# Performance work log

Hardware: AMD Instinct MI355X
Metric: run time of the kernel (lower is better)

## Reference

```python
import jax, jax.numpy as jnp
import numpy as np

N_NODES = 50000
N_EDGES = 800000
F = 128
LN_EPS = 1e-5


def _sage_conv(h, src, dst, Wl, bl, Wr, n_nodes):
    # PyG SAGEConv (aggr='mean', root_weight=True):
    #   out_i = lin_l(mean_{j->i} h_j) + lin_r(h_i)
    msg = h[src]  # [E, F] irregular gather
    s = jax.ops.segment_sum(msg, dst, num_segments=n_nodes)  # [N, F]
    deg = jax.ops.segment_sum(jnp.ones((src.shape[0],), h.dtype), dst,
                              num_segments=n_nodes)  # [N]
    mean = s / jnp.maximum(deg, 1.0)[:, None]
    return mean @ Wl.T + bl + h @ Wr.T


def _graph_layernorm(h, w, b):
    # PyG LayerNorm mode='graph', batch=None: normalize over ALL entries,
    # eps added to std, then per-channel affine.
    m = h.mean()
    std = jnp.sqrt(jnp.mean((h - m) ** 2))
    return (h - m) / (std + LN_EPS) * w + b


def _prelu(h, w):
    # nn.PReLU(1): single shared slope
    return jnp.where(h >= 0, h, w * h)


def setup_inputs() -> dict:
    key = jax.random.key(0)
    ks = jax.random.split(key, 12)
    sc = 1.0 / np.sqrt(F)
    x = jax.random.normal(ks[0], (N_NODES, F), dtype=jnp.float32)
    edge_index = jax.random.randint(ks[1], (2, N_EDGES), 0, N_NODES, dtype=jnp.int64)
    return {
        "x": x,
        "edge_index": edge_index,
        "Wl0": jax.random.uniform(ks[2], (F, F), jnp.float32, -sc, sc),
        "bl0": jnp.zeros((F,), jnp.float32),
        "Wr0": jax.random.uniform(ks[3], (F, F), jnp.float32, -sc, sc),
        "ln_w0": jnp.ones((F,), jnp.float32),
        "ln_b0": jnp.zeros((F,), jnp.float32),
        "pw0": jnp.full((1,), 0.25, jnp.float32),
        "skipW0": jax.random.uniform(ks[4], (F, F), jnp.float32, -sc, sc),
        "Wl1": jax.random.uniform(ks[5], (F, F), jnp.float32, -sc, sc),
        "bl1": jnp.zeros((F,), jnp.float32),
        "Wr1": jax.random.uniform(ks[6], (F, F), jnp.float32, -sc, sc),
        "ln_w1": jnp.ones((F,), jnp.float32),
        "ln_b1": jnp.zeros((F,), jnp.float32),
        "pw1": jnp.full((1,), 0.25, jnp.float32),
    }


def reference(x, edge_index, Wl0, bl0, Wr0, ln_w0, ln_b0, pw0, skipW0,
              Wl1, bl1, Wr1, ln_w1, ln_b1, pw1):
    src, dst = edge_index[0], edge_index[1]
    n = x.shape[0]
    # layer 0: h = x
    h = _sage_conv(x, src, dst, Wl0, bl0, Wr0, n)
    h = _graph_layernorm(h, ln_w0, ln_b0)
    h1 = _prelu(h, pw0)
    # layer 1: h = skip(x) + h1
    h = x @ skipW0.T + h1
    h = _sage_conv(h, src, dst, Wl1, bl1, Wr1, n)
    h = _graph_layernorm(h, ln_w1, ln_b1)
    h = _prelu(h, pw1)
    return h
```

## Files before the change

kernel.cpp:

```cpp
#include <hip/hip_runtime.h>

#define LN_EPS 1e-5f
#define BUCKCAP 4096
#define PCHUNK 6656
#define PK 13

typedef short bf16x8 __attribute__((ext_vector_type(8)));
typedef float f32x4  __attribute__((ext_vector_type(4)));

static __device__ __forceinline__ float4 ld4(const float* p){ return *(const float4*)p; }
static __device__ __forceinline__ uint f2bf1(float f){
  uint u = __float_as_uint(f);
  return (u + 0x7fffu + ((u >> 16) & 1u)) >> 16;
}
static __device__ __forceinline__ float bf2f(uint lo16){ return __uint_as_float(lo16 << 16); }

__global__ void detect_fmt_kernel(const int* __restrict__ ei, int* __restrict__ flag){
  __shared__ int any;
  if (threadIdx.x == 0) any = 0;
  __syncthreads();
  int nz = 0;
  for (int i = threadIdx.x; i < 1024; i += 256)
    nz |= (ei[2*i+1] != 0);
  if (nz) atomicOr(&any, 1);
  __syncthreads();
  if (threadIdx.x == 0) *flag = any;
}

__global__ __launch_bounds__(512) void partition_kernel(
    const int* __restrict__ ei, int E, const int* __restrict__ flag,
    int* __restrict__ bucket_count, uint* __restrict__ ebuf, int nbuck){
  __shared__ int hist[512];
  __shared__ int base[512];
  __shared__ int cur[512];
  const int tid = threadIdx.x;
  const int lo = blockIdx.x * PCHUNK;
  const int hi = min(lo + PCHUNK, E);
  hist[tid] = 0;
  __syncthreads();

  const int fmt = *flag;
  uint pd[PK];
  #pragma unroll
  for (int k = 0; k < PK; k++){
    int e = lo + tid + k*512;
    uint v = 0xffffffffu;
    if (e < hi){
      int s, d;
      if (fmt){ s = ei[e]; d = ei[E + e]; }
      else    { s = ei[2*e]; d = ei[2*(E + e)]; }
      v = ((uint)d << 16) | (uint)s;
      atomicAdd(&hist[v >> 23], 1);
    }
    pd[k] = v;
  }
  __syncthreads();
  { int h = hist[tid];
    base[tid] = (h > 0 && tid < nbuck) ? atomicAdd(&bucket_count[tid], h) : 0;
    cur[tid] = 0; }
  __syncthreads();
  #pragma unroll
  for (int k = 0; k < PK; k++){
    int e = lo + tid + k*512;
    if (e < hi){
      uint v = pd[k];
      int b = v >> 23;
      int pos = base[b] + atomicAdd(&cur[b], 1);
      if (pos < BUCKCAP) ebuf[(size_t)b*BUCKCAP + pos] = v;
    }
  }
}

__global__ void convert_bf16_kernel(const float* __restrict__ src, ushort* __restrict__ dst, int n8){
  int i = blockIdx.x*256 + threadIdx.x;
  if (i >= n8) return;
  float4 a = ld4(src + (size_t)i*8);
  float4 b = ld4(src + (size_t)i*8 + 4);
  uint4 o;
  o.x = f2bf1(a.x) | (f2bf1(a.y) << 16);
  o.y = f2bf1(a.z) | (f2bf1(a.w) << 16);
  o.z = f2bf1(b.x) | (f2bf1(b.y) << 16);
  o.w = f2bf1(b.z) | (f2bf1(b.w) << 16);
  *(uint4*)(dst + (size_t)i*8) = o;
}

__global__ void convert_w_kernel(const float* __restrict__ s0, const float* __restrict__ s1,
                                 const float* __restrict__ s2, const float* __restrict__ s3,
                                 const float* __restrict__ s4, ushort* __restrict__ dst){
  int i = blockIdx.x*256 + threadIdx.x;
  if (i >= 10240) return;
  int m = i >> 11;
  int o = (i & 2047) * 8;
  const float* s = (m == 0) ? s0 : (m == 1) ? s1 : (m == 2) ? s2 : (m == 3) ? s3 : s4;
  float4 a = ld4(s + o);
  float4 b = ld4(s + o + 4);
  uint4 v;
  v.x = f2bf1(a.x) | (f2bf1(a.y) << 16);
  v.y = f2bf1(a.z) | (f2bf1(a.w) << 16);
  v.z = f2bf1(b.x) | (f2bf1(b.y) << 16);
  v.w = f2bf1(b.z) | (f2bf1(b.w) << 16);
  *(uint4*)(dst + (size_t)m*16384 + o) = v;
}

__global__ __launch_bounds__(512) void bucket_aggregate(const ushort* __restrict__ h,
    const uint* __restrict__ ebuf, const int* __restrict__ bucket_count,
    ushort* __restrict__ outmean, int N){
  __shared__ ushort ssrc[BUCKCAP];
  __shared__ int lcnt[128], lofs[128], lcur[128];
  const int tid = threadIdx.x;
  const int b = blockIdx.x;
  const int n0 = b << 7;
  const uint* eb = ebuf + (size_t)b*BUCKCAP;
  const int cnt = min(bucket_count[b], BUCKCAP);

  if (tid < 128) lcnt[tid] = 0;
  __syncthreads();
  for (int e = tid; e < cnt; e += 512)
    atomicAdd(&lcnt[(eb[e] >> 16) & 127], 1);
  __syncthreads();
  if (tid < 128){
    int v = lcnt[tid];
    int s = v;
    #pragma unroll
    for (int off = 1; off < 64; off <<= 1){
      int u = __shfl_up(s, off);
      if ((tid & 63) >= off) s += u;
    }
    lofs[tid] = s - v;
  }
  __syncthreads();
  if (tid >= 64 && tid < 128)
    lofs[tid] += lofs[63] + lcnt[63];
  __syncthreads();
  if (tid < 128) lcur[tid] = lofs[tid];
  __syncthreads();
  for (int e = tid; e < cnt; e += 512){
    uint v = eb[e];
    int pos = atomicAdd(&lcur[(v >> 16) & 127], 1);
    ssrc[pos] = (ushort)(v & 0xffffu);
  }
  __syncthreads();

  const int wv = tid >> 6, lane = tid & 63;
  const uint* hp = (const uint*)h;
  uint* op = (uint*)outmean;
  #pragma unroll 1
  for (int i = 0; i < 16; i++){
    int j = wv*16 + i;
    int node = n0 + j;
    if (node >= N) break;
    int start = lofs[j];
    int d = lcnt[j];
    float ax = 0.f, ay = 0.f;
    int e = 0;
    for (; e + 4 <= d; e += 4){
      int s0 = ssrc[start+e+0], s1 = ssrc[start+e+1];
      int s2 = ssrc[start+e+2], s3 = ssrc[start+e+3];
      uint v0 = hp[(size_t)s0*64 + lane];
      uint v1 = hp[(size_t)s1*64 + lane];
      uint v2 = hp[(size_t)s2*64 + lane];
      uint v3 = hp[(size_t)s3*64 + lane];
      ax += bf2f(v0 & 0xffffu) + bf2f(v1 & 0xffffu) + bf2f(v2 & 0xffffu) + bf2f(v3 & 0xffffu);
      ay += bf2f(v0 >> 16) + bf2f(v1 >> 16) + bf2f(v2 >> 16) + bf2f(v3 >> 16);
    }
    for (; e < d; e++){
      int s0 = ssrc[start+e];
      uint v = hp[(size_t)s0*64 + lane];
      ax += bf2f(v & 0xffffu);
      ay += bf2f(v >> 16);
    }
    float inv = 1.f / fmaxf((float)d, 1.f);
    op[(size_t)node*64 + lane] = f2bf1(ax*inv) | (f2bf1(ay*inv) << 16);
  }
}

__global__ __launch_bounds__(256) void gemm_dual_mfma(
    const ushort* __restrict__ A1, const ushort* __restrict__ A2,
    const ushort* __restrict__ W1, const ushort* __restrict__ W2,
    const float* __restrict__ bias, float* __restrict__ out,
    int N, double* __restrict__ stats){
  const int tid  = threadIdx.x;
  const int lane = tid & 63;
  const int wv   = tid >> 6;
  const int r0   = blockIdx.x*128 + wv*32;
  const int lrow = lane & 15;
  const int lk   = (lane >> 4) * 8;

  f32x4 acc[2][8] = {};

  #pragma unroll
  for (int ks = 0; ks < 4; ks++){
    const int kb = ks*32 + lk;
    bf16x8 a1[2], a2[2];
    #pragma unroll
    for (int m = 0; m < 2; m++){
      int r = r0 + m*16 + lrow;
      if (r > N-1) r = N-1;
      a1[m] = *(const bf16x8*)(A1 + (size_t)r*128 + kb);
      a2[m] = *(const bf16x8*)(A2 + (size_t)r*128 + kb);
    }
    #pragma unroll
    for (int n = 0; n < 8; n++){
      const int c = n*16 + lrow;
      bf16x8 b1 = *(const bf16x8*)(W1 + c*128 + kb);
      bf16x8 b2 = *(const bf16x8*)(W2 + c*128 + kb);
      #pragma unroll
      for (int m = 0; m < 2; m++){
        acc[m][n] = __builtin_amdgcn_mfma_f32_16x16x32_bf16(a1[m], b1, acc[m][n], 0, 0, 0);
        acc[m][n] = __builtin_amdgcn_mfma_f32_16x16x32_bf16(a2[m], b2, acc[m][n], 0, 0, 0);
      }
    }
  }

  float bn[8];
  #pragma unroll
  for (int n = 0; n < 8; n++) bn[n] = bias[n*16 + lrow];

  double ls1 = 0.0, ls2 = 0.0;
  const int rb = (lane >> 4) * 4;
  #pragma unroll
  for (int m = 0; m < 2; m++){
    #pragma unroll
    for (int j = 0; j < 4; j++){
      int r = r0 + m*16 + rb + j;
      if (r < N){
        #pragma unroll
        for (int n = 0; n < 8; n++){
          float v = acc[m][n][j] + bn[n];
          out[(size_t)r*128 + n*16 + lrow] = v;
          ls1 += (double)v;
          ls2 += (double)v * (double)v;
        }
      }
    }
  }
  #pragma unroll
  for (int off = 32; off > 0; off >>= 1){
    ls1 += __shfl_down(ls1, off);
    ls2 += __shfl_down(ls2, off);
  }
  __shared__ double red[8];
  if (lane == 0){ red[wv*2] = ls1; red[wv*2+1] = ls2; }
  __syncthreads();
  if (tid == 0) atomicAdd(&stats[0], red[0]+red[2]+red[4]+red[6]);
  if (tid == 1) atomicAdd(&stats[1], red[1]+red[3]+red[5]+red[7]);
}

__global__ __launch_bounds__(256) void gemm_skip_mfma(
    const ushort* __restrict__ A, const ushort* __restrict__ W,
    const float* __restrict__ T0, const double* __restrict__ stats,
    const float* __restrict__ lnw, const float* __restrict__ lnb,
    const float* __restrict__ pw,
    ushort* __restrict__ outb, int N, double inv_cnt){
  const int tid  = threadIdx.x;
  const int lane = tid & 63;
  const int wv   = tid >> 6;
  const int r0   = blockIdx.x*128 + wv*32;
  const int lrow = lane & 15;
  const int lk   = (lane >> 4) * 8;

  f32x4 acc[2][8] = {};

  #pragma unroll
  for (int ks = 0; ks < 4; ks++){
    const int kb = ks*32 + lk;
    bf16x8 a[2];
    #pragma unroll
    for (int m = 0; m < 2; m++){
      int r = r0 + m*16 + lrow;
      if (r > N-1) r = N-1;
      a[m] = *(const bf16x8*)(A + (size_t)r*128 + kb);
    }
    #pragma unroll
    for (int n = 0; n < 8; n++){
      const int c = n*16 + lrow;
      bf16x8 b = *(const bf16x8*)(W + c*128 + kb);
      #pragma unroll
      for (int m = 0; m < 2; m++)
        acc[m][n] = __builtin_amdgcn_mfma_f32_16x16x32_bf16(a[m], b, acc[m][n], 0, 0, 0);
    }
  }

  double s1 = stats[0], s2 = stats[1];
  double md = s1 * inv_cnt;
  double var = s2 * inv_cnt - md*md;
  float mean = (float)md;
  float rstd = 1.f / ((float)sqrt(fmax(var, 0.0)) + LN_EPS);
  float slope = pw[0];
  float wn[8], bb[8];
  #pragma unroll
  for (int n = 0; n < 8; n++){
    wn[n] = lnw[n*16 + lrow];
    bb[n] = lnb[n*16 + lrow];
  }

  const int rb = (lane >> 4) * 4;
  #pragma unroll
  for (int m = 0; m < 2; m++){
    #pragma unroll
    for (int j = 0; j < 4; j++){
      int r = r0 + m*16 + rb + j;
      if (r < N){
        #pragma unroll
        for (int n = 0; n < 8; n++){
          float t = T0[(size_t)r*128 + n*16 + lrow];
          float l = (t - mean)*rstd*wn[n] + bb[n];
          l = (l >= 0.f) ? l : slope*l;
          float v = acc[m][n][j] + l;
          outb[(size_t)r*128 + n*16 + lrow] = (ushort)f2bf1(v);
        }
      }
    }
  }
}

__global__ __launch_bounds__(256) void ln_prelu_kernel(
    const float* __restrict__ T, const double* __restrict__ stats,
    const float* __restrict__ lnw, const float* __restrict__ lnb,
    const float* __restrict__ pw, float* __restrict__ out,
    int nf4, double inv_cnt){
  double s1 = stats[0], s2 = stats[1];
  double md = s1 * inv_cnt;
  double var = s2 * inv_cnt - md*md;
  float mean = (float)md;
  float rstd = 1.f / ((float)sqrt(fmax(var, 0.0)) + LN_EPS);
  float slope = pw[0];
  for (int i = blockIdx.x*256 + threadIdx.x; i < nf4; i += gridDim.x*256){
    int c4 = i & 31;
    float4 t = ld4(T + (size_t)i*4);
    float4 w4 = ld4(lnw + c4*4);
    float4 b4 = ld4(lnb + c4*4);
    float4 v; float l;
    l = (t.x - mean)*rstd*w4.x + b4.x; v.x = (l >= 0.f ? l : slope*l);
    l = (t.y - mean)*rstd*w4.y + b4.y; v.y = (l >= 0.f ? l : slope*l);
    l = (t.z - mean)*rstd*w4.z + b4.z; v.z = (l >= 0.f ? l : slope*l);
    l = (t.w - mean)*rstd*w4.w + b4.w; v.w = (l >= 0.f ? l : slope*l);
    *(float4*)(out + (size_t)i*4) = v;
  }
}

extern "C" void kernel_launch(void* const* d_in, const int* in_sizes, int n_in,
                              void* d_out, int out_size, void* d_ws, size_t ws_size,
                              hipStream_t stream){
  const float* x    = (const float*)d_in[0];
  const int*   ei   = (const int*)d_in[1];
  const float* Wl0  = (const float*)d_in[2];
  const float* bl0  = (const float*)d_in[3];
  const float* Wr0  = (const float*)d_in[4];
  const float* lnw0 = (const float*)d_in[5];
  const float* lnb0 = (const float*)d_in[6];
  const float* pw0  = (const float*)d_in[7];
  const float* skW  = (const float*)d_in[8];
  const float* Wl1  = (const float*)d_in[9];
  const float* bl1  = (const float*)d_in[10];
  const float* Wr1  = (const float*)d_in[11];
  const float* lnw1 = (const float*)d_in[12];
  const float* lnb1 = (const float*)d_in[13];
  const float* pw1  = (const float*)d_in[14];

  const int N = in_sizes[0] / 128;
  const int E = in_sizes[1] / 2;

  char* p = (char*)d_ws;
  auto carve = [&](size_t bytes)->char*{
    char* r = p;
    p += (bytes + 255) & ~(size_t)255;
    return r;
  };
  double* stats   = (double*)carve(4*sizeof(double));
  int*    flag    = (int*)carve(sizeof(int));
  int*    bcnt    = (int*)carve((size_t)512*4);
  uint*   ebuf    = (uint*)carve((size_t)512*BUCKCAP*4);
  ushort* x16     = (ushort*)carve((size_t)N*128*2);
  ushort* mean16  = (ushort*)carve((size_t)N*128*2);
  ushort* hskip16 = (ushort*)carve((size_t)N*128*2);
  ushort* wbuf    = (ushort*)carve((size_t)5*16384*2);
  float*  tbuf    = (float*)d_out;

  ushort* Wl0_16 = wbuf;
  ushort* Wr0_16 = wbuf + 16384;
  ushort* skW_16 = wbuf + 32768;
  ushort* Wl1_16 = wbuf + 49152;
  ushort* Wr1_16 = wbuf + 65536;

  hipMemsetAsync(stats, 0, 4*sizeof(double), stream);
  hipMemsetAsync(bcnt, 0, 512*4, stream);

  const int nbuck = (N + 127) >> 7;
  const int pb = (E + PCHUNK - 1) / PCHUNK;
  detect_fmt_kernel<<<1, 256, 0, stream>>>(ei, flag);
  partition_kernel<<<pb, 512, 0, stream>>>(ei, E, flag, bcnt, ebuf, nbuck);
  convert_bf16_kernel<<<(N*16 + 255)/256, 256, 0, stream>>>(x, x16, N*16);
  convert_w_kernel<<<40, 256, 0, stream>>>(Wl0, Wr0, skW, Wl1, Wr1, wbuf);

  int gb = (N + 127)/128;
  double inv_cnt = 1.0 / ((double)N * 128.0);

  bucket_aggregate<<<nbuck, 512, 0, stream>>>(x16, ebuf, bcnt, mean16, N);
  gemm_dual_mfma<<<gb, 256, 0, stream>>>(mean16, x16, Wl0_16, Wr0_16, bl0, tbuf, N, stats);
  gemm_skip_mfma<<<gb, 256, 0, stream>>>(x16, skW_16, tbuf, stats, lnw0, lnb0, pw0, hskip16, N, inv_cnt);
  bucket_aggregate<<<nbuck, 512, 0, stream>>>(hskip16, ebuf, bcnt, mean16, N);
  gemm_dual_mfma<<<gb, 256, 0, stream>>>(mean16, hskip16, Wl1_16, Wr1_16, bl1, tbuf, N, stats + 2);
  ln_prelu_kernel<<<2048, 256, 0, stream>>>(tbuf, stats + 2, lnw1, lnb1, pw1, (float*)d_out, N*32, inv_cnt);
}
```

Measured before the change: 287.6 us.

## Halve bucket size to 64 nodes, fold memsets into detect kernel, unroll gather by 8

Edges are now partitioned into 1024 buckets of 64 destination nodes, keyed on the top bits of the packed dst<<16 word, with the per-bucket capacity halved. This doubles the number of aggregation blocks so more CUs are kept busy, and it shortens the shared-memory prefix scan. The two hipMemsetAsync calls are replaced by zeroing stats and bucket counts inside the format-detect kernel, which saves launches. The gather loop is unrolled to 8 loads in flight to hide more latency, at some cost in register pressure. Bucket capacity of 2048 with an average of about 1024 edges per bucket leaves less headroom before edges are silently dropped.

```diff
diff --git a/kernel.cpp b/kernel.cpp
--- a/kernel.cpp
+++ b/kernel.cpp
@@ -1,7 +1,7 @@
 #include <hip/hip_runtime.h>
 
 #define LN_EPS 1e-5f
-#define BUCKCAP 4096
+#define BUCKCAP 2048
 #define PCHUNK 6656
 #define PK 13
 
@@ -15,7 +15,8 @@
 }
 static __device__ __forceinline__ float bf2f(uint lo16){ return __uint_as_float(lo16 << 16); }
 
-__global__ void detect_fmt_kernel(const int* __restrict__ ei, int* __restrict__ flag){
+__global__ void detect_fmt_kernel(const int* __restrict__ ei, int* __restrict__ flag,
+                                  double* __restrict__ stats, int* __restrict__ bcnt){
   __shared__ int any;
   if (threadIdx.x == 0) any = 0;
   __syncthreads();
@@ -23,20 +24,22 @@
   for (int i = threadIdx.x; i < 1024; i += 256)
     nz |= (ei[2*i+1] != 0);
   if (nz) atomicOr(&any, 1);
+  for (int i = threadIdx.x; i < 1024; i += 256) bcnt[i] = 0;
+  if (threadIdx.x < 4) stats[threadIdx.x] = 0.0;
   __syncthreads();
   if (threadIdx.x == 0) *flag = any;
 }
 
 __global__ __launch_bounds__(512) void partition_kernel(
     const int* __restrict__ ei, int E, const int* __restrict__ flag,
-    int* __restrict__ bucket_count, uint* __restrict__ ebuf, int nbuck){
-  __shared__ int hist[512];
-  __shared__ int base[512];
-  __shared__ int cur[512];
+    int* __restrict__ bucket_count, uint* __restrict__ ebuf){
+  __shared__ int hist[1024];
+  __shared__ int base[1024];
+  __shared__ int cur[1024];
   const int tid = threadIdx.x;
   const int lo = blockIdx.x * PCHUNK;
   const int hi = min(lo + PCHUNK, E);
-  hist[tid] = 0;
+  hist[tid] = 0; hist[tid + 512] = 0;
   __syncthreads();
 
   const int fmt = *flag;
@@ -50,21 +53,25 @@
       if (fmt){ s = ei[e]; d = ei[E + e]; }
       else    { s = ei[2*e]; d = ei[2*(E + e)]; }
       v = ((uint)d << 16) | (uint)s;
-      atomicAdd(&hist[v >> 23], 1);
+      atomicAdd(&hist[v >> 22], 1);
     }
     pd[k] = v;
   }
   __syncthreads();
-  { int h = hist[tid];
-    base[tid] = (h > 0 && tid < nbuck) ? atomicAdd(&bucket_count[tid], h) : 0;
-    cur[tid] = 0; }
+  #pragma unroll
+  for (int t0 = 0; t0 < 2; t0++){
+    int t = tid + t0*512;
+    int h = hist[t];
+    base[t] = (h > 0) ? atomicAdd(&bucket_count[t], h) : 0;
+    cur[t] = 0;
+  }
   __syncthreads();
   #pragma unroll
   for (int k = 0; k < PK; k++){
     int e = lo + tid + k*512;
     if (e < hi){
       uint v = pd[k];
-      int b = v >> 23;
+      int b = v >> 22;
       int pos = base[b] + atomicAdd(&cur[b], 1);
       if (pos < BUCKCAP) ebuf[(size_t)b*BUCKCAP + pos] = v;
     }
@@ -106,37 +113,33 @@
     const uint* __restrict__ ebuf, const int* __restrict__ bucket_count,
     ushort* __restrict__ outmean, int N){
   __shared__ ushort ssrc[BUCKCAP];
-  __shared__ int lcnt[128], lofs[128], lcur[128];
+  __shared__ int lcnt[64], lofs[64], lcur[64];
   const int tid = threadIdx.x;
   const int b = blockIdx.x;
-  const int n0 = b << 7;
+  const int n0 = b << 6;
   const uint* eb = ebuf + (size_t)b*BUCKCAP;
   const int cnt = min(bucket_count[b], BUCKCAP);
 
-  if (tid < 128) lcnt[tid] = 0;
+  if (tid < 64) lcnt[tid] = 0;
   __syncthreads();
   for (int e = tid; e < cnt; e += 512)
-    atomicAdd(&lcnt[(eb[e] >> 16) & 127], 1);
-  __syncthreads();
-  if (tid < 128){
+    atomicAdd(&lcnt[(eb[e] >> 16) & 63], 1);
+  __syncthreads();
+  if (tid < 64){
     int v = lcnt[tid];
     int s = v;
     #pragma unroll
     for (int off = 1; off < 64; off <<= 1){
       int u = __shfl_up(s, off);
-      if ((tid & 63) >= off) s += u;
+      if (tid >= off) s += u;
     }
     lofs[tid] = s - v;
-  }
-  __syncthreads();
-  if (tid >= 64 && tid < 128)
-    lofs[tid] += lofs[63] + lcnt[63];
-  __syncthreads();
-  if (tid < 128) lcur[tid] = lofs[tid];
+    lcur[tid] = s - v;
+  }
   __syncthreads();
   for (int e = tid; e < cnt; e += 512){
     uint v = eb[e];
-    int pos = atomicAdd(&lcur[(v >> 16) & 127], 1);
+    int pos = atomicAdd(&lcur[(v >> 16) & 63], 1);
     ssrc[pos] = (ushort)(v & 0xffffu);
   }
   __syncthreads();
@@ -145,27 +148,30 @@
   const uint* hp = (const uint*)h;
   uint* op = (uint*)outmean;
   #pragma unroll 1
-  for (int i = 0; i < 16; i++){
-    int j = wv*16 + i;
+  for (int i = 0; i < 8; i++){
+    int j = wv*8 + i;
     int node = n0 + j;
     if (node >= N) break;
     int start = lofs[j];
     int d = lcnt[j];
     float ax = 0.f, ay = 0.f;
     int e = 0;
-    for (; e + 4 <= d; e += 4){
-      int s0 = ssrc[start+e+0], s1 = ssrc[start+e+1];
-      int s2 = ssrc[start+e+2], s3 = ssrc[start+e+3];
-      uint v0 = hp[(size_t)s0*64 + lane];
-      uint v1 = hp[(size_t)s1*64 + lane];
-      uint v2 = hp[(size_t)s2*64 + lane];
-      uint v3 = hp[(size_t)s3*64 + lane];
-      ax += bf2f(v0 & 0xffffu) + bf2f(v1 & 0xffffu) + bf2f(v2 & 0xffffu) + bf2f(v3 & 0xffffu);
-      ay += bf2f(v0 >> 16) + bf2f(v1 >> 16) + bf2f(v2 >> 16) + bf2f(v3 >> 16);
+    for (; e + 8 <= d; e += 8){
+      uint v0 = hp[(size_t)ssrc[start+e+0]*64 + lane];
+      uint v1 = hp[(size_t)ssrc[start+e+1]*64 + lane];
+      uint v2 = hp[(size_t)ssrc[start+e+2]*64 + lane];
+      uint v3 = hp[(size_t)ssrc[start+e+3]*64 + lane];
+      uint v4 = hp[(size_t)ssrc[start+e+4]*64 + lane];
+      uint v5 = hp[(size_t)ssrc[start+e+5]*64 + lane];
+      uint v6 = hp[(size_t)ssrc[start+e+6]*64 + lane];
+      uint v7 = hp[(size_t)ssrc[start+e+7]*64 + lane];
+      ax += bf2f(v0 & 0xffffu) + bf2f(v1 & 0xffffu) + bf2f(v2 & 0xffffu) + bf2f(v3 & 0xffffu)
+          + bf2f(v4 & 0xffffu) + bf2f(v5 & 0xffffu) + bf2f(v6 & 0xffffu) + bf2f(v7 & 0xffffu);
+      ay += bf2f(v0 >> 16) + bf2f(v1 >> 16) + bf2f(v2 >> 16) + bf2f(v3 >> 16)
+          + bf2f(v4 >> 16) + bf2f(v5 >> 16) + bf2f(v6 >> 16) + bf2f(v7 >> 16);
     }
     for (; e < d; e++){
-      int s0 = ssrc[start+e];
-      uint v = hp[(size_t)s0*64 + lane];
+      uint v = hp[(size_t)ssrc[start+e]*64 + lane];
       ax += bf2f(v & 0xffffu);
       ay += bf2f(v >> 16);
     }
@@ -369,8 +375,8 @@
   };
   double* stats   = (double*)carve(4*sizeof(double));
   int*    flag    = (int*)carve(sizeof(int));
-  int*    bcnt    = (int*)carve((size_t)512*4);
-  uint*   ebuf    = (uint*)carve((size_t)512*BUCKCAP*4);
+  int*    bcnt    = (int*)carve((size_t)1024*4);
+  uint*   ebuf    = (uint*)carve((size_t)1024*BUCKCAP*4);
   ushort* x16     = (ushort*)carve((size_t)N*128*2);
   ushort* mean16  = (ushort*)carve((size_t)N*128*2);
   ushort* hskip16 = (ushort*)carve((size_t)N*128*2);
@@ -383,13 +389,10 @@
   ushort* Wl1_16 = wbuf + 49152;
   ushort* Wr1_16 = wbuf + 65536;
 
-  hipMemsetAsync(stats, 0, 4*sizeof(double), stream);
-  hipMemsetAsync(bcnt, 0, 512*4, stream);
-
-  const int nbuck = (N + 127) >> 7;
+  const int nbuck = (N + 63) >> 6;
   const int pb = (E + PCHUNK - 1) / PCHUNK;
-  detect_fmt_kernel<<<1, 256, 0, stream>>>(ei, flag);
-  partition_kernel<<<pb, 512, 0, stream>>>(ei, E, flag, bcnt, ebuf, nbuck);
+  detect_fmt_kernel<<<1, 256, 0, stream>>>(ei, flag, stats, bcnt);
+  partition_kernel<<<pb, 512, 0, stream>>>(ei, E, flag, bcnt, ebuf);
   convert_bf16_kernel<<<(N*16 + 255)/256, 256, 0, stream>>>(x, x16, N*16);
   convert_w_kernel<<<40, 256, 0, stream>>>(Wl0, Wr0, skW, Wl1, Wr1, wbuf);
 
```

Measured after the change: 269.6 us. 1.07x faster.
